# Kernel tuning notes

Hardware: AMD Instinct MI355X
Metric: run time of the kernel (lower is better)

Reference implementation:

```python
import jax, jax.numpy as jnp
import numpy as np

B, T, E, A = 4, 4096, 1024, 1024

def setup_inputs() -> dict:
    key = jax.random.key(0)
    k1, k2, k3, k4 = jax.random.split(key, 4)
    scale = 1.0 / np.sqrt(E)  # ~ nn.Linear default init scale
    return {
        "embedded": jax.random.normal(k1, (B, T, E), dtype=jnp.float32),
        "Wq": jax.random.uniform(k2, (A, E), jnp.float32, -scale, scale),
        "Wk": jax.random.uniform(k3, (A, E), jnp.float32, -scale, scale),
        "Wv": jax.random.uniform(k4, (A, E), jnp.float32, -scale, scale),
    }

def reference(embedded, Wq, Wk, Wv):
    # QKV projections (nn.Linear without bias: x @ W.T)
    q = jnp.einsum('bte,ae->bta', embedded, Wq)
    k = jnp.einsum('bte,ae->bta', embedded, Wk)
    v = jnp.einsum('bte,ae->bta', embedded, Wv)
    A_dim = q.shape[-1]
    # scaled scores [B, T, T]
    scores = jnp.einsum('bqa,bka->bqk', q, k) / jnp.sqrt(jnp.float32(A_dim))
    # causal mask (lower triangular allowed)
    Tq = scores.shape[-1]
    causal = jnp.tril(jnp.ones((Tq, Tq), dtype=bool))
    scores = jnp.where(causal, scores, -jnp.inf)
    probs = jax.nn.softmax(scores, axis=-1)
    out = jnp.einsum('bqk,bka->bqa', probs, v)
    return jnp.round(out, 4)
```

## Files before the change

kernel.cpp:

```cpp
#include <hip/hip_runtime.h>
#include <hip/hip_bf16.h>

using bf16 = __hip_bfloat16;

typedef __attribute__((ext_vector_type(4))) float f32x4;
typedef __attribute__((ext_vector_type(8))) short short8;

typedef const void __attribute__((address_space(1)))* gas1_t;
typedef void __attribute__((address_space(3)))* las3_t;
#define GLDS(gp, lp) __builtin_amdgcn_global_load_lds((gas1_t)(gp), (las3_t)(lp), 16, 0, 0)

__device__ inline short f2bfbits(float f) {
  union { bf16 h; short s; } u;
  u.h = __float2bfloat16(f);
  return u.s;
}
__device__ inline float bf2f(short u) {
  unsigned x = ((unsigned)(unsigned short)u) << 16;
  float f; __builtin_memcpy(&f, &x, 4); return f;
}

__device__ inline void store_out(float* C, size_t idx, float v) { C[idx] = v; }
__device__ inline void store_out(bf16* C, size_t idx, float v) { C[idx] = __float2bfloat16(v); }

template<typename TOUT, int MODE>
__global__ __launch_bounds__(512, 2) void gemm256(
    const short* __restrict__ A, int lda, size_t sAz,
    const short* __restrict__ B, int ldb, size_t sBz,
    TOUT* __restrict__ C, int ldc, size_t sCz,
    int K, float scale)
{
  int bx, by;
  if constexpr (MODE == 1) {
    const int i = blockIdx.x;
    by = (int)((__builtin_sqrtf(8.f * (float)i + 1.f) - 1.f) * 0.5f);
    if (((by * (by + 1)) >> 1) > i) by--;
    else if ((((by + 1) * (by + 2)) >> 1) <= i) by++;
    bx = i - ((by * (by + 1)) >> 1);
  } else {
    bx = blockIdx.x; by = blockIdx.y;
  }
  const int z = blockIdx.z;
  const int tri_by = (by * (by + 1)) >> 1;

  A += (size_t)z * sAz;
  B += (size_t)z * sBz;
  C += (size_t)z * sCz;

  const int NT = K >> 5;

  __shared__ short As[3][256 * 32];
  __shared__ short Bs[3][256 * 32];

  const int t = threadIdx.x;
  const int lane = t & 63;
  const int wave = t >> 6;
  const int wm = wave >> 2;
  const int wn = wave & 3;
  const int fr = lane & 15, kh = lane >> 4;
  const int koff = ((kh ^ ((fr >> 1) & 3)) << 3);

  int srow[2], scol[2];
  #pragma unroll
  for (int j = 0; j < 2; j++) {
    int e = j * 512 + t;
    srow[j] = e >> 2;
    scol[j] = (((e & 3) ^ ((e >> 3) & 3)) << 3);
  }

  f32x4 acc[8][4];
  #pragma unroll
  for (int i = 0; i < 8; i++)
    #pragma unroll
    for (int j = 0; j < 4; j++) acc[i][j] = (f32x4){0.f, 0.f, 0.f, 0.f};

  auto STAGE_A = [&](int kt) {
    const int buf = kt % 3, k0 = kt * 32;
    #pragma unroll
    for (int j = 0; j < 2; j++) {
      const short* pa = A + (size_t)(by * 256 + srow[j]) * lda + k0 + scol[j];
      GLDS(pa, (char*)&As[buf][0] + j * 8192 + wave * 1024);
    }
  };
  auto STAGE_B = [&](int kt) {
    const int buf = kt % 3, k0 = kt * 32;
    #pragma unroll
    for (int j = 0; j < 2; j++) {
      const short* pb = B + (size_t)(bx * 256 + srow[j]) * ldb + k0 + scol[j];
      GLDS(pb, (char*)&Bs[buf][0] + j * 8192 + wave * 1024);
    }
  };

  STAGE_A(0); STAGE_B(0);
  STAGE_A(1); STAGE_B(1);
  asm volatile("s_waitcnt vmcnt(4)\ns_barrier" ::: "memory");

  const int arow = wm * 128 + fr;
  const int brow = wn * 64 + fr;

  for (int kt = 0; kt < NT; kt++) {
    const short* as = &As[kt % 3][0];
    const short* bs = &Bs[kt % 3][0];
    short8 af[4], bfr[4];

    #pragma unroll
    for (int n = 0; n < 4; n++) bfr[n] = *(const short8*)&bs[(brow + n * 16) * 32 + koff];
    #pragma unroll
    for (int m = 0; m < 4; m++) af[m] = *(const short8*)&as[(arow + m * 16) * 32 + koff];
    if (kt + 2 < NT) STAGE_A(kt + 2);
    __builtin_amdgcn_s_barrier();
    asm volatile("s_waitcnt lgkmcnt(0)" ::: "memory");
    __builtin_amdgcn_sched_barrier(0);
    __builtin_amdgcn_s_setprio(1);
    #pragma unroll
    for (int m = 0; m < 4; m++)
      #pragma unroll
      for (int n = 0; n < 4; n++)
        acc[m][n] = __builtin_amdgcn_mfma_f32_16x16x32_bf16(af[m], bfr[n], acc[m][n], 0, 0, 0);
    __builtin_amdgcn_s_setprio(0);
    __builtin_amdgcn_sched_barrier(0);

    #pragma unroll
    for (int m = 0; m < 4; m++) af[m] = *(const short8*)&as[(arow + (m + 4) * 16) * 32 + koff];
    if (kt + 2 < NT) STAGE_B(kt + 2);
    __builtin_amdgcn_s_barrier();
    asm volatile("s_waitcnt lgkmcnt(0)" ::: "memory");
    __builtin_amdgcn_sched_barrier(0);
    __builtin_amdgcn_s_setprio(1);
    #pragma unroll
    for (int m = 0; m < 4; m++)
      #pragma unroll
      for (int n = 0; n < 4; n++)
        acc[m + 4][n] = __builtin_amdgcn_mfma_f32_16x16x32_bf16(af[m], bfr[n], acc[m + 4][n], 0, 0, 0);
    __builtin_amdgcn_s_setprio(0);
    __builtin_amdgcn_sched_barrier(0);

    if (kt + 2 < NT)      asm volatile("s_waitcnt vmcnt(4)\ns_barrier" ::: "memory");
    else if (kt + 1 < NT) asm volatile("s_waitcnt vmcnt(0)\ns_barrier" ::: "memory");
  }

  #pragma unroll
  for (int m = 0; m < 8; m++)
    #pragma unroll
    for (int n = 0; n < 4; n++) {
      int col_l = wn * 64 + n * 16 + fr;
      #pragma unroll
      for (int r = 0; r < 4; r++) {
        int row_l = wm * 128 + m * 16 + kh * 4 + r;
        if constexpr (MODE == 1)
          store_out(C, (size_t)(tri_by + bx) * 65536 + (size_t)row_l * 256 + col_l,
                    acc[m][n][r] * scale);
        else
          store_out(C, (size_t)(by * 256 + row_l) * ldc + bx * 256 + col_l,
                    acc[m][n][r] * scale);
      }
    }
}

__global__ __launch_bounds__(256, 2) void gemm_pv(
    const short* __restrict__ SP, const short* __restrict__ Vt,
    float* __restrict__ Out)
{
  const int w = blockIdx.x;
  const int k = w >> 8, c = w & 255;
  const int bx = c & 7;
  const int g = (c >> 3) & 7;
  const int z = c >> 6;
  const int by = k ? 15 - g : g;
  const int tri_by = (by * (by + 1)) >> 1;

  const short* A = SP + (size_t)z * 136 * 65536;
  const int Klen = (by + 1) * 256;
  const int NT = Klen >> 5;

  __shared__ short As[2][256 * 32];
  __shared__ short Bs[2][128 * 32];

  const int t = threadIdx.x;
  const int lane = t & 63;
  const int wave = t >> 6;
  const int wm = wave >> 1;
  const int wn = wave & 1;
  const int fr = lane & 15, kh = lane >> 4;
  const int koff = ((kh ^ ((fr >> 1) & 3)) << 3);

  f32x4 acc[8][4];
  #pragma unroll
  for (int i = 0; i < 8; i++)
    #pragma unroll
    for (int j = 0; j < 4; j++) acc[i][j] = (f32x4){0.f, 0.f, 0.f, 0.f};

  auto STAGE_A = [&](int kt) {
    const int buf = kt & 1, k0 = kt * 32;
    #pragma unroll
    for (int j = 0; j < 4; j++) {
      int e = j * 256 + t;
      int row = e >> 2;
      int sc = (((e & 3) ^ ((row >> 1) & 3)) << 3);
      const short* pa = A + (size_t)(tri_by + (k0 >> 8)) * 65536
                          + (size_t)row * 256 + (k0 & 255) + sc;
      GLDS(pa, (char*)&As[buf][0] + j * 4096 + wave * 1024);
    }
  };
  auto STAGE_B = [&](int kt) {
    const int buf = kt & 1, k0 = kt * 32;
    #pragma unroll
    for (int j = 0; j < 2; j++) {
      int e = j * 256 + t;
      int row = e >> 2;
      int sc = (((e & 3) ^ ((row >> 1) & 3)) << 3);
      const short* pb = Vt + (size_t)(bx * 128 + row) * 16384 + z * 4096 + k0 + sc;
      GLDS(pb, (char*)&Bs[buf][0] + j * 4096 + wave * 1024);
    }
  };

  STAGE_A(0); STAGE_B(0);
  asm volatile("s_waitcnt vmcnt(0)\ns_barrier" ::: "memory");

  const int arow = wm * 128 + fr;
  const int brow = wn * 64 + fr;

  for (int kt = 0; kt < NT; kt++) {
    const short* as = &As[kt & 1][0];
    const short* bs = &Bs[kt & 1][0];
    short8 af[4], bfr[4];

    #pragma unroll
    for (int n = 0; n < 4; n++) bfr[n] = *(const short8*)&bs[(brow + n * 16) * 32 + koff];
    #pragma unroll
    for (int m = 0; m < 4; m++) af[m] = *(const short8*)&as[(arow + m * 16) * 32 + koff];
    if (kt + 1 < NT) STAGE_A(kt + 1);
    asm volatile("s_waitcnt lgkmcnt(0)" ::: "memory");
    __builtin_amdgcn_sched_barrier(0);
    __builtin_amdgcn_s_setprio(1);
    #pragma unroll
    for (int m = 0; m < 4; m++)
      #pragma unroll
      for (int n = 0; n < 4; n++)
        acc[m][n] = __builtin_amdgcn_mfma_f32_16x16x32_bf16(af[m], bfr[n], acc[m][n], 0, 0, 0);
    __builtin_amdgcn_s_setprio(0);
    __builtin_amdgcn_sched_barrier(0);

    #pragma unroll
    for (int m = 0; m < 4; m++) af[m] = *(const short8*)&as[(arow + (m + 4) * 16) * 32 + koff];
    if (kt + 1 < NT) STAGE_B(kt + 1);
    asm volatile("s_waitcnt lgkmcnt(0)" ::: "memory");
    __builtin_amdgcn_sched_barrier(0);
    __builtin_amdgcn_s_setprio(1);
    #pragma unroll
    for (int m = 0; m < 4; m++)
      #pragma unroll
      for (int n = 0; n < 4; n++)
        acc[m + 4][n] = __builtin_amdgcn_mfma_f32_16x16x32_bf16(af[m], bfr[n], acc[m + 4][n], 0, 0, 0);
    __builtin_amdgcn_s_setprio(0);
    __builtin_amdgcn_sched_barrier(0);

    if (kt + 1 < NT)
      asm volatile("s_waitcnt vmcnt(0)\ns_barrier" ::: "memory");
  }

  float* Cz = Out + (size_t)z * 4096 * 1024;
  #pragma unroll
  for (int m = 0; m < 8; m++)
    #pragma unroll
    for (int n = 0; n < 4; n++) {
      int col = bx * 128 + wn * 64 + n * 16 + fr;
      #pragma unroll
      for (int r = 0; r < 4; r++) {
        int row_l = wm * 128 + m * 16 + kh * 4 + r;
        Cz[(size_t)(by * 256 + row_l) * 1024 + col] = acc[m][n][r];
      }
    }
}

__global__ __launch_bounds__(256) void gemm128(
    const short* __restrict__ A, int lda,
    const short* __restrict__ B, int ldb,
    bf16* __restrict__ C, int ldc, int K, float scale)
{
  const int bx = blockIdx.x, by = blockIdx.y;
  __shared__ short a_lds[128 * 32];
  __shared__ short b_lds[128 * 32];

  const int t = threadIdx.x;
  const int lane = t & 63;
  const int wave = t >> 6;
  const int wm = wave >> 1, wn = wave & 1;
  const int fr = lane & 15, kh = lane >> 4;

  f32x4 acc[4][4];
  #pragma unroll
  for (int i = 0; i < 4; i++)
    #pragma unroll
    for (int j = 0; j < 4; j++) acc[i][j] = (f32x4){0.f, 0.f, 0.f, 0.f};

  for (int k0 = 0; k0 < K; k0 += 32) {
    #pragma unroll
    for (int i = 0; i < 2; i++) {
      int e = i * 256 + t;
      int r_ = e >> 2, c_ = (e & 3) * 8;
      GLDS(A + (size_t)(by * 128 + r_) * lda + k0 + c_, (char*)a_lds + i * 4096 + wave * 1024);
      GLDS(B + (size_t)(bx * 128 + r_) * ldb + k0 + c_, (char*)b_lds + i * 4096 + wave * 1024);
    }
    __syncthreads();

    short8 af[4], bfr[4];
    #pragma unroll
    for (int m = 0; m < 4; m++)
      af[m] = *(const short8*)&a_lds[(wm * 64 + m * 16 + fr) * 32 + kh * 8];
    #pragma unroll
    for (int n = 0; n < 4; n++)
      bfr[n] = *(const short8*)&b_lds[(wn * 64 + n * 16 + fr) * 32 + kh * 8];
    #pragma unroll
    for (int m = 0; m < 4; m++)
      #pragma unroll
      for (int n = 0; n < 4; n++)
        acc[m][n] = __builtin_amdgcn_mfma_f32_16x16x32_bf16(af[m], bfr[n], acc[m][n], 0, 0, 0);
    __syncthreads();
  }

  #pragma unroll
  for (int m = 0; m < 4; m++)
    #pragma unroll
    for (int n = 0; n < 4; n++) {
      int col = bx * 128 + wn * 64 + n * 16 + fr;
      #pragma unroll
      for (int r = 0; r < 4; r++) {
        int row = by * 128 + wm * 64 + m * 16 + kh * 4 + r;
        C[(size_t)row * ldc + col] = __float2bfloat16(acc[m][n][r] * scale);
      }
    }
}

__global__ __launch_bounds__(256) void cvt_bf16(
    const float* __restrict__ in, bf16* __restrict__ out, int n, float scale)
{
  for (int i = (blockIdx.x * 256 + threadIdx.x) * 8; i < n; i += gridDim.x * 2048) {
    f32x4 v0 = *(const f32x4*)&in[i];
    f32x4 v1 = *(const f32x4*)&in[i + 4];
    short8 o = { f2bfbits(v0[0] * scale), f2bfbits(v0[1] * scale),
                 f2bfbits(v0[2] * scale), f2bfbits(v0[3] * scale),
                 f2bfbits(v1[0] * scale), f2bfbits(v1[1] * scale),
                 f2bfbits(v1[2] * scale), f2bfbits(v1[3] * scale) };
    *(short8*)&out[i] = o;
  }
}

__global__ __launch_bounds__(256) void cvt_t_bf16(
    const float* __restrict__ in, bf16* __restrict__ out, int N)
{
  __shared__ float tile[64][65];
  const int bx = blockIdx.x, by = blockIdx.y;
  const int t = threadIdx.x;
  #pragma unroll
  for (int i = 0; i < 16; i++) {
    int e = i * 256 + t;
    int r = e >> 6, c = e & 63;
    tile[r][c] = in[(size_t)(by * 64 + r) * N + bx * 64 + c];
  }
  __syncthreads();
  #pragma unroll
  for (int i = 0; i < 16; i++) {
    int e = i * 256 + t;
    int r = e >> 6, c = e & 63;
    out[(size_t)(bx * 64 + r) * N + by * 64 + c] = __float2bfloat16(tile[c][r]);
  }
}

__global__ __launch_bounds__(256) void softmax_causal_packed(short* SP, int T)
{
  __shared__ float rowv[4096];
  __shared__ float red[4];
  const int r = blockIdx.x;
  const int z = blockIdx.y;
  const int rb = r >> 8, rl = r & 255;
  const size_t tri = (size_t)((rb * (rb + 1)) >> 1);
  short* base = SP + (size_t)z * 136 * 65536;
  const int L = r + 1;
  const int kend = (rb + 1) * 256;
  const int t = threadIdx.x;

  float lmax = -3.0e38f;
  for (int i = t * 8; i < kend; i += 2048) {
    short8 s = *(const short8*)(base + (tri + (i >> 8)) * 65536 + (size_t)rl * 256 + (i & 255));
    #pragma unroll
    for (int j = 0; j < 8; j++) {
      float v = bf2f(s[j]);
      rowv[i + j] = v;
      if (i + j < L) lmax = fmaxf(lmax, v);
    }
  }
  #pragma unroll
  for (int o = 32; o > 0; o >>= 1) lmax = fmaxf(lmax, __shfl_down(lmax, o));
  if ((t & 63) == 0) red[t >> 6] = lmax;
  __syncthreads();
  const float m = fmaxf(fmaxf(red[0], red[1]), fmaxf(red[2], red[3]));
  __syncthreads();

  float lsum = 0.f;
  for (int i = t; i < kend; i += 256) {
    float e = (i < L) ? __expf(rowv[i] - m) : 0.f;
    rowv[i] = e;
    lsum += e;
  }
  #pragma unroll
  for (int o = 32; o > 0; o >>= 1) lsum += __shfl_down(lsum, o);
  if ((t & 63) == 0) red[t >> 6] = lsum;
  __syncthreads();
  const float inv = 1.f / (red[0] + red[1] + red[2] + red[3]);

  for (int i = t * 8; i < kend; i += 2048) {
    short8 o;
    #pragma unroll
    for (int j = 0; j < 8; j++) o[j] = f2bfbits(rowv[i + j] * inv);
    *(short8*)(base + (tri + (i >> 8)) * 65536 + (size_t)rl * 256 + (i & 255)) = o;
  }
}

extern "C" void kernel_launch(void* const* d_in, const int* in_sizes, int n_in,
                              void* d_out, int out_size, void* d_ws, size_t ws_size,
                              hipStream_t stream) {
  (void)in_sizes; (void)n_in; (void)out_size; (void)ws_size;
  const float* X  = (const float*)d_in[0];
  const float* Wq = (const float*)d_in[1];
  const float* Wk = (const float*)d_in[2];
  const float* Wv = (const float*)d_in[3];
  float* Out = (float*)d_out;

  const int Bn = 4, T = 4096, E = 1024, Ad = 1024;
  const int M = Bn * T;

  char* ws = (char*)d_ws;
  short* Q2  = (short*)ws;
  short* Vt  = (short*)(ws + 33554432);
  short* Xb  = (short*)(ws + 67108864);
  short* WqT = (short*)(ws + 100663296);
  short* WkT = (short*)(ws + 102760448);
  short* Wvb = (short*)(ws + 104857600);
  short* W2T = (short*)(ws + 106954752);
  short* SP  = (short*)(ws + 109051904);

  dim3 blk(256), blk5(512);
  const size_t SPz = (size_t)136 * 65536;

  cvt_bf16<<<dim3(8192), blk, 0, stream>>>(X, (bf16*)Xb, M * E, 1.0f);
  cvt_t_bf16<<<dim3(16, 16), blk, 0, stream>>>(Wq, (bf16*)WqT, E);
  cvt_t_bf16<<<dim3(16, 16), blk, 0, stream>>>(Wk, (bf16*)WkT, E);
  cvt_bf16<<<dim3(512), blk, 0, stream>>>(Wv, (bf16*)Wvb, Ad * E, 1.0f);

  gemm128<<<dim3(8, 8), blk, 0, stream>>>(
      WkT, Ad, WqT, Ad, (bf16*)W2T, E, Ad, 0.03125f);

  gemm256<bf16, 0><<<dim3(1024 / 256, M / 256), blk5, 0, stream>>>(
      Xb, E, 0, W2T, E, 0, (bf16*)Q2, 1024, 0, E, 1.0f);

  gemm256<bf16, 0><<<dim3(M / 256, Ad / 256), blk5, 0, stream>>>(
      Wvb, E, 0, Xb, E, 0, (bf16*)Vt, M, 0, E, 1.0f);

  gemm256<bf16, 1><<<dim3(136, 1, Bn), blk5, 0, stream>>>(
      Q2, 1024, (size_t)T * 1024,
      Xb, 1024, (size_t)T * 1024,
      (bf16*)SP, 256, SPz, E, 1.0f);

  softmax_causal_packed<<<dim3(T, Bn), blk, 0, stream>>>(SP, T);

  gemm_pv<<<dim3(512), blk, 0, stream>>>(SP, Vt, Out);
}
```

Baseline: 384.4 us.

## Split long causal PV rows across two blocks with 256x256 tiles and reduce

Replaces the PV GEMM with 512-thread blocks that compute 256x256 output tiles. Row tiles in the lower (longer) half of the causal triangle have their K range split into two halves, giving 384 roughly balanced blocks. The second half writes fp32 partials into workspace that reuses the Q2 region, and a separate reduce kernel adds them into the output. Staging moves to a 3-buffer pipeline with two tiles in flight, at the cost of extra partial-sum traffic, an extra launch, and more LDS per block.

```diff
diff --git a/kernel.cpp b/kernel.cpp
--- a/kernel.cpp
+++ b/kernel.cpp
@@ -157,33 +157,48 @@
     }
 }
 
-__global__ __launch_bounds__(256, 2) void gemm_pv(
+__global__ __launch_bounds__(512, 2) void gemm_pv_split(
     const short* __restrict__ SP, const short* __restrict__ Vt,
-    float* __restrict__ Out)
+    float* __restrict__ Out, float* __restrict__ Ppart)
 {
   const int w = blockIdx.x;
-  const int k = w >> 8, c = w & 255;
-  const int bx = c & 7;
-  const int g = (c >> 3) & 7;
-  const int z = c >> 6;
-  const int by = k ? 15 - g : g;
+  int by, bx, z, kt0, kt1, u;
+  bool topart;
+  if (w < 128) {
+    by = w & 7; bx = (w >> 3) & 3; z = w >> 5;
+    kt0 = 0; kt1 = (by + 1) * 8; topart = false; u = 0;
+  } else {
+    const int v = w - 128;
+    const int h = v & 1;
+    u = v >> 1;
+    by = 8 + (u & 7); bx = (u >> 3) & 3; z = u >> 5;
+    const int n = (by + 1) * 8, half = n >> 1;
+    kt0 = h ? half : 0;
+    kt1 = h ? n : half;
+    topart = (h == 1);
+  }
   const int tri_by = (by * (by + 1)) >> 1;
-
   const short* A = SP + (size_t)z * 136 * 65536;
-  const int Klen = (by + 1) * 256;
-  const int NT = Klen >> 5;
-
-  __shared__ short As[2][256 * 32];
-  __shared__ short Bs[2][128 * 32];
+
+  __shared__ short As[3][256 * 32];
+  __shared__ short Bs[3][256 * 32];
 
   const int t = threadIdx.x;
   const int lane = t & 63;
   const int wave = t >> 6;
-  const int wm = wave >> 1;
-  const int wn = wave & 1;
+  const int wm = wave >> 2;
+  const int wn = wave & 3;
   const int fr = lane & 15, kh = lane >> 4;
   const int koff = ((kh ^ ((fr >> 1) & 3)) << 3);
 
+  int srow[2], scol[2];
+  #pragma unroll
+  for (int j = 0; j < 2; j++) {
+    int e = j * 512 + t;
+    srow[j] = e >> 2;
+    scol[j] = (((e & 3) ^ ((e >> 3) & 3)) << 3);
+  }
+
   f32x4 acc[8][4];
   #pragma unroll
   for (int i = 0; i < 8; i++)
@@ -191,45 +206,41 @@
     for (int j = 0; j < 4; j++) acc[i][j] = (f32x4){0.f, 0.f, 0.f, 0.f};
 
   auto STAGE_A = [&](int kt) {
-    const int buf = kt & 1, k0 = kt * 32;
-    #pragma unroll
-    for (int j = 0; j < 4; j++) {
-      int e = j * 256 + t;
-      int row = e >> 2;
-      int sc = (((e & 3) ^ ((row >> 1) & 3)) << 3);
+    const int buf = kt % 3, k0 = kt * 32;
+    #pragma unroll
+    for (int j = 0; j < 2; j++) {
       const short* pa = A + (size_t)(tri_by + (k0 >> 8)) * 65536
-                          + (size_t)row * 256 + (k0 & 255) + sc;
-      GLDS(pa, (char*)&As[buf][0] + j * 4096 + wave * 1024);
+                          + (size_t)srow[j] * 256 + (k0 & 255) + scol[j];
+      GLDS(pa, (char*)&As[buf][0] + j * 8192 + wave * 1024);
     }
   };
   auto STAGE_B = [&](int kt) {
-    const int buf = kt & 1, k0 = kt * 32;
+    const int buf = kt % 3, k0 = kt * 32;
     #pragma unroll
     for (int j = 0; j < 2; j++) {
-      int e = j * 256 + t;
-      int row = e >> 2;
-      int sc = (((e & 3) ^ ((row >> 1) & 3)) << 3);
-      const short* pb = Vt + (size_t)(bx * 128 + row) * 16384 + z * 4096 + k0 + sc;
-      GLDS(pb, (char*)&Bs[buf][0] + j * 4096 + wave * 1024);
+      const short* pb = Vt + (size_t)(bx * 256 + srow[j]) * 16384 + z * 4096 + k0 + scol[j];
+      GLDS(pb, (char*)&Bs[buf][0] + j * 8192 + wave * 1024);
     }
   };
 
-  STAGE_A(0); STAGE_B(0);
-  asm volatile("s_waitcnt vmcnt(0)\ns_barrier" ::: "memory");
+  STAGE_A(kt0); STAGE_B(kt0);
+  STAGE_A(kt0 + 1); STAGE_B(kt0 + 1);
+  asm volatile("s_waitcnt vmcnt(4)\ns_barrier" ::: "memory");
 
   const int arow = wm * 128 + fr;
   const int brow = wn * 64 + fr;
 
-  for (int kt = 0; kt < NT; kt++) {
-    const short* as = &As[kt & 1][0];
-    const short* bs = &Bs[kt & 1][0];
+  for (int kt = kt0; kt < kt1; kt++) {
+    const short* as = &As[kt % 3][0];
+    const short* bs = &Bs[kt % 3][0];
     short8 af[4], bfr[4];
 
     #pragma unroll
     for (int n = 0; n < 4; n++) bfr[n] = *(const short8*)&bs[(brow + n * 16) * 32 + koff];
     #pragma unroll
     for (int m = 0; m < 4; m++) af[m] = *(const short8*)&as[(arow + m * 16) * 32 + koff];
-    if (kt + 1 < NT) STAGE_A(kt + 1);
+    if (kt + 2 < kt1) STAGE_A(kt + 2);
+    __builtin_amdgcn_s_barrier();
     asm volatile("s_waitcnt lgkmcnt(0)" ::: "memory");
     __builtin_amdgcn_sched_barrier(0);
     __builtin_amdgcn_s_setprio(1);
@@ -243,7 +254,8 @@
 
     #pragma unroll
     for (int m = 0; m < 4; m++) af[m] = *(const short8*)&as[(arow + (m + 4) * 16) * 32 + koff];
-    if (kt + 1 < NT) STAGE_B(kt + 1);
+    if (kt + 2 < kt1) STAGE_B(kt + 2);
+    __builtin_amdgcn_s_barrier();
     asm volatile("s_waitcnt lgkmcnt(0)" ::: "memory");
     __builtin_amdgcn_sched_barrier(0);
     __builtin_amdgcn_s_setprio(1);
@@ -255,22 +267,45 @@
     __builtin_amdgcn_s_setprio(0);
     __builtin_amdgcn_sched_barrier(0);
 
-    if (kt + 1 < NT)
-      asm volatile("s_waitcnt vmcnt(0)\ns_barrier" ::: "memory");
-  }
-
-  float* Cz = Out + (size_t)z * 4096 * 1024;
+    if (kt + 2 < kt1)      asm volatile("s_waitcnt vmcnt(4)\ns_barrier" ::: "memory");
+    else if (kt + 1 < kt1) asm volatile("s_waitcnt vmcnt(0)\ns_barrier" ::: "memory");
+  }
+
   #pragma unroll
   for (int m = 0; m < 8; m++)
     #pragma unroll
     for (int n = 0; n < 4; n++) {
-      int col = bx * 128 + wn * 64 + n * 16 + fr;
+      int col_l = wn * 64 + n * 16 + fr;
       #pragma unroll
       for (int r = 0; r < 4; r++) {
         int row_l = wm * 128 + m * 16 + kh * 4 + r;
-        Cz[(size_t)(by * 256 + row_l) * 1024 + col] = acc[m][n][r];
+        if (topart)
+          Ppart[(size_t)u * 65536 + (size_t)row_l * 256 + col_l] = acc[m][n][r];
+        else
+          Out[(size_t)z * 4096 * 1024 + (size_t)(by * 256 + row_l) * 1024
+              + bx * 256 + col_l] = acc[m][n][r];
       }
     }
+}
+
+__global__ __launch_bounds__(256) void pv_reduce(
+    const float* __restrict__ Ppart, float* __restrict__ Out)
+{
+  const int u = blockIdx.x;
+  const int rg = blockIdx.y;
+  const int by = 8 + (u & 7), bx = (u >> 3) & 3, z = u >> 5;
+  const int t = threadIdx.x;
+  const float* src = Ppart + (size_t)u * 65536 + (size_t)rg * 32 * 256;
+  float* dst = Out + (size_t)z * 4096 * 1024
+                   + (size_t)(by * 256 + rg * 32) * 1024 + bx * 256;
+  for (int i = t * 4; i < 8192; i += 1024) {
+    int row = i >> 8, col = i & 255;
+    f32x4 a = *(const f32x4*)&src[i];
+    float* d = &dst[(size_t)row * 1024 + col];
+    f32x4 b = *(const f32x4*)d;
+    b[0] += a[0]; b[1] += a[1]; b[2] += a[2]; b[3] += a[3];
+    *(f32x4*)d = b;
+  }
 }
 
 __global__ __launch_bounds__(256) void gemm128(
@@ -439,6 +474,7 @@
   short* Wvb = (short*)(ws + 104857600);
   short* W2T = (short*)(ws + 106954752);
   short* SP  = (short*)(ws + 109051904);
+  float* Ppart = (float*)ws;
 
   dim3 blk(256), blk5(512);
   const size_t SPz = (size_t)136 * 65536;
@@ -464,5 +500,6 @@
 
   softmax_causal_packed<<<dim3(T, Bn), blk, 0, stream>>>(SP, T);
 
-  gemm_pv<<<dim3(512), blk, 0, stream>>>(SP, Vt, Out);
-}
+  gemm_pv_split<<<dim3(384), blk5, 0, stream>>>(SP, Vt, Out, Ppart);
+  pv_reduce<<<dim3(128, 8), blk, 0, stream>>>(Ppart, Out);
+}
```

New measurement: 407.5 us. 1.06x slower.
